# Kernel tuning notes

Hardware: AMD Instinct MI355X
Metric: run time of the kernel (lower is better)

The kernel has to match this reference:

```python
import jax, jax.numpy as jnp
import numpy as np

VOCAB = 32000
EMB = 512
UNITS = 1024
B, T = 128, 256


def setup_inputs() -> dict:
    key = jax.random.key(0)
    ks = jax.random.split(key, 9)
    s = 0.05
    return {
        "tokens": jax.random.randint(ks[0], (B, T), 0, VOCAB),
        "emb_table": jax.random.normal(ks[1], (VOCAB, EMB), jnp.float32) * s,
        "Wx_f": jax.random.normal(ks[2], (EMB, 3 * UNITS), jnp.float32) * s,
        "Wh_f": jax.random.normal(ks[3], (UNITS, 3 * UNITS), jnp.float32) * s,
        "b_f": jnp.zeros((2, 3 * UNITS), jnp.float32),  # [input_bias, recurrent_bias] (reset_after=True)
        "Wx_b": jax.random.normal(ks[4], (EMB, 3 * UNITS), jnp.float32) * s,
        "Wh_b": jax.random.normal(ks[5], (UNITS, 3 * UNITS), jnp.float32) * s,
        "b_b": jnp.zeros((2, 3 * UNITS), jnp.float32),
        "fc_W": jax.random.normal(ks[6], (2 * UNITS, UNITS), jnp.float32) * s,
        "fc_b": jnp.zeros((UNITS,), jnp.float32),
    }


def _gru_dir(x_proj, mask, Wh, b_rec, reverse):
    # x_proj: [B,T,3U] precomputed input projections (z|r|h gate order, Keras),
    # mask: [B,T] bool. Keras GRU v2 semantics: reset_after=True,
    # sigmoid recurrent activation, tanh activation; masked steps carry state.
    b, u = x_proj.shape[0], Wh.shape[0]

    def step(h, inputs):
        xp, m = inputs  # [B,3U], [B]
        rec = h @ Wh + b_rec  # [B,3U]
        xz, xr, xh = jnp.split(xp, 3, axis=-1)
        rz, rr, rh = jnp.split(rec, 3, axis=-1)
        z = jax.nn.sigmoid(xz + rz)
        r = jax.nn.sigmoid(xr + rr)
        hh = jnp.tanh(xh + r * rh)
        h_new = z * h + (1.0 - z) * hh
        h_new = jnp.where(m[:, None], h_new, h)
        return h_new, h_new

    h0 = jnp.zeros((b, u), x_proj.dtype)
    xs = (jnp.swapaxes(x_proj, 0, 1), jnp.swapaxes(mask, 0, 1))  # time-major
    h_last, outs = jax.lax.scan(step, h0, xs, reverse=reverse)
    return jnp.swapaxes(outs, 0, 1), h_last  # [B,T,U], [B,U]


def reference(tokens, emb_table, Wx_f, Wh_f, b_f, Wx_b, Wh_b, b_b, fc_W, fc_b):
    mask = tokens != 0  # Embedding(mask_zero=True)
    x = emb_table[tokens]  # [B,T,E]
    xp_f = x @ Wx_f + b_f[0]
    xp_b = x @ Wx_b + b_b[0]
    out_f, h_f = _gru_dir(xp_f, mask, Wh_f, b_f[1], reverse=False)
    out_b, h_b = _gru_dir(xp_b, mask, Wh_b, b_b[1], reverse=True)
    output = jnp.concatenate([out_f, out_b], axis=-1)  # [B,T,2U]
    hidden = jnp.concatenate([h_f, h_b], axis=-1) @ fc_W + fc_b  # [B,U]
    return output, hidden
```

## Files before the change

### kernel.cpp

```cpp
#include <hip/hip_runtime.h>


#define T_SEQ 256
#define BATCH 128
#define EMB_D 512
#define UNITS 1024
#define NROWS (BATCH * T_SEQ)
#define N3U 3072
#define N6U 6144
#define XT_STRIDE 786432
#define HSTR (BATCH * 2048)
#define HROT 16

#define SBAR()      __builtin_amdgcn_s_barrier()
#define SCHED0()    __builtin_amdgcn_sched_barrier(0)
#define WAIT_LGKM() asm volatile("s_waitcnt lgkmcnt(0)" ::: "memory")
#define WAIT_VM()   asm volatile("s_waitcnt vmcnt(0)" ::: "memory")

typedef __attribute__((ext_vector_type(8))) __bf16 bfv8;
typedef __attribute__((ext_vector_type(4))) float f32x4;

__device__ inline unsigned short f2bf(float f) {
  union { float f; unsigned int u; } x; x.f = f;
  unsigned int u = x.u;
  unsigned int r = (u + 0x7fffu + ((u >> 16) & 1u)) >> 16;
  return (unsigned short)r;
}
__device__ inline float bf2f(unsigned short h) {
  union { unsigned int u; float f; } x; x.u = ((unsigned int)h) << 16;
  return x.f;
}
__device__ inline f32x4 mfma16(bfv8 a, bfv8 b, f32x4 c) {
  return __builtin_amdgcn_mfma_f32_16x16x32_bf16(a, b, c, 0, 0, 0);
}
__device__ inline void gl_lds16(const unsigned short* g, unsigned short* l) {
  __builtin_amdgcn_global_load_lds(
      (const __attribute__((address_space(1))) void*)g,
      (__attribute__((address_space(3))) void*)l, 16, 0, 0);
}

__global__ __launch_bounds__(256) void k_transpose(const float* __restrict__ src,
                                                   unsigned short* __restrict__ dst,
                                                   int K, int N) {
  __shared__ float tile[32][33];
  int k0 = blockIdx.x * 32, n0 = blockIdx.y * 32;
  int tx = threadIdx.x & 31, ty = threadIdx.x >> 5;
#pragma unroll
  for (int i = 0; i < 4; ++i)
    tile[ty + i * 8][tx] = src[(size_t)(k0 + ty + i * 8) * N + n0 + tx];
  __syncthreads();
#pragma unroll
  for (int i = 0; i < 4; ++i)
    dst[(size_t)(n0 + ty + i * 8) * K + k0 + tx] = f2bf(tile[tx][ty + i * 8]);
}

__global__ __launch_bounds__(256) void k_gather(const int* __restrict__ tokens,
                                                const float* __restrict__ emb,
                                                unsigned short* __restrict__ Xbf) {
  int idx = blockIdx.x * 256 + threadIdx.x;
  int row = idx >> 7;
  int c4 = (idx & 127) * 4;
  int tok = tokens[row];
  float4 v = *(const float4*)(emb + (size_t)tok * EMB_D + c4);
  ushort4 p;
  p.x = f2bf(v.x); p.y = f2bf(v.y); p.z = f2bf(v.z); p.w = f2bf(v.w);
  *(ushort4*)(Xbf + (size_t)row * EMB_D + c4) = p;
}

__global__ __launch_bounds__(256) void k_bias(const float* __restrict__ bf_,
                                              const float* __restrict__ bb_,
                                              float* __restrict__ biasX,
                                              float* __restrict__ biasH) {
  int i = blockIdx.x * 256 + threadIdx.x;
  if (i >= N6U) return;
  if (i < N3U) { biasX[i] = bf_[i];        biasH[i] = bf_[N3U + i]; }
  else         { biasX[i] = bb_[i - N3U];  biasH[i] = bb_[i]; }
}

__global__ __launch_bounds__(256) void k_tokt(const int* __restrict__ tokens,
                                              int* __restrict__ tokT) {
  int i = blockIdx.x * 256 + threadIdx.x;
  int b = i >> 8, t = i & 255;
  tokT[t * BATCH + b] = tokens[i];
}

__global__ __launch_bounds__(256) void k_gemm(const unsigned short* __restrict__ A,
                                              const unsigned short* __restrict__ BT,
                                              const float* __restrict__ bias,
                                              void* __restrict__ C,
                                              int M, int N, int K, int mode) {
  __shared__ unsigned short As[128 * 32];
  __shared__ unsigned short Bs[128 * 32];
  const int mt = blockIdx.x, nt = blockIdx.y;
  const int tid = threadIdx.x;
  const int wid = tid >> 6, lane = tid & 63;
  const int wm = (wid >> 1) * 64, wn = (wid & 1) * 64;
  const int l15 = lane & 15, lk = (lane >> 4) * 8;

  f32x4 acc[4][4];
#pragma unroll
  for (int i = 0; i < 4; ++i)
#pragma unroll
    for (int j = 0; j < 4; ++j) acc[i][j] = (f32x4){0.f, 0.f, 0.f, 0.f};

  const int r = tid >> 2;
  const int cc = (tid & 3) * 8;
  const unsigned short* ga0 = A + (size_t)(mt * 128 + r) * K + cc;
  const unsigned short* ga1 = ga0 + (size_t)64 * K;
  const unsigned short* gb0 = BT + (size_t)(nt * 128 + r) * K + cc;
  const unsigned short* gb1 = gb0 + (size_t)64 * K;
  unsigned short* lA0 = As + r * 32 + cc;
  unsigned short* lA1 = As + (64 + r) * 32 + cc;
  unsigned short* lB0 = Bs + r * 32 + cc;
  unsigned short* lB1 = Bs + (64 + r) * 32 + cc;

  for (int k0 = 0; k0 < K; k0 += 32) {
    __syncthreads();
    gl_lds16(ga0 + k0, lA0);
    gl_lds16(ga1 + k0, lA1);
    gl_lds16(gb0 + k0, lB0);
    gl_lds16(gb1 + k0, lB1);
    __syncthreads();
    bfv8 af[4], bfr[4];
#pragma unroll
    for (int i = 0; i < 4; ++i) {
      af[i]  = *(const bfv8*)(As + (wm + i * 16 + l15) * 32 + lk);
      bfr[i] = *(const bfv8*)(Bs + (wn + i * 16 + l15) * 32 + lk);
    }
#pragma unroll
    for (int i = 0; i < 4; ++i)
#pragma unroll
      for (int j = 0; j < 4; ++j) acc[i][j] = mfma16(af[i], bfr[j], acc[i][j]);
  }

#pragma unroll
  for (int j = 0; j < 4; ++j) {
    const int col = nt * 128 + wn + j * 16 + l15;
    const float bv = bias[col];
    const int dirc = (col >= N3U) ? 1 : 0;
    const int cm = col - dirc * N3U;
    const int g = cm >> 10;
    const int uu = cm & 1023;
    const size_t cbase = (size_t)dirc * 393216 + (size_t)(uu >> 4) * 6144 +
                         (size_t)g * 16 + (uu & 15);
#pragma unroll
    for (int i = 0; i < 4; ++i) {
      const int row0 = mt * 128 + wm + i * 16 + (lane >> 4) * 4;
#pragma unroll
      for (int q = 0; q < 4; ++q) {
        const float v = acc[i][j][q] + bv;
        const int row = row0 + q;
        if (mode == 1) {
          ((float*)C)[(size_t)row * N + col] = v;
        } else {
          const int b = row >> 8, tt = row & 255;
          ((unsigned short*)C)[(size_t)tt * XT_STRIDE + cbase + (size_t)b * 48] = f2bf(v);
        }
      }
    }
  }
}

__global__ __launch_bounds__(256) void k_scan(const unsigned short* __restrict__ XPn,
                                              const unsigned short* __restrict__ WhT,
                                              const float* __restrict__ biasH,
                                              const int* __restrict__ tokT,
                                              unsigned short* __restrict__ hbR,
                                              float* __restrict__ out,
                                              unsigned int* __restrict__ bar) {
  __shared__ unsigned short Wl[3 * 128 * 16 * 8];
  __shared__ unsigned short xb[64 * 48];
  __shared__ int tkb[64];
  __shared__ unsigned short bounce[64 * 24];

  const int bid = blockIdx.x;
  const int grp = bid & 3;
  const int dir = grp >> 1;
  const int mg  = grp & 1;
  const int ut  = bid >> 2;
  const int u0 = ut * 16, m0 = mg * 64;
  const int sub = ut & 7;
  const int tid = threadIdx.x;

  for (int c = tid; c < 6144; c += 256) {
    const int g  = c >> 11;
    const int kb = (c >> 4) & 127;
    const int uu = c & 15;
    *(uint4*)(Wl + (((g << 7) | kb) * 16 + uu) * 8) =
        *(const uint4*)(WhT + (((size_t)(dir * N3U + (g << 10) + u0 + uu)) << 10) + (kb << 3));
  }

  const int lane = tid & 63, wid = tid >> 6;
  const int l15 = lane & 15, hi = lane >> 4;
  const size_t aoff = ((size_t)(m0 + wid * 16 + l15) << 11) + (dir << 10) + (hi << 3);
  const int u = u0 + l15;
  const float bz  = biasH[dir * N3U + u];
  const float brg = biasH[dir * N3U + 1024 + u];
  const float bhg = biasH[dir * N3U + 2048 + u];
  const int rb = wid * 16 + (hi << 2);
  const int ob = m0 + rb;
  const size_t woff = (dir << 10) + u;
  const int sr = tid >> 2, sc4 = (tid & 3) << 2;
  const size_t soff = ((size_t)(m0 + sr) << 11) + (dir << 10) + u0 + sc4;

  const unsigned short* xpb = XPn + (size_t)dir * 393216 + (size_t)ut * 6144 + (size_t)m0 * 48;

  unsigned long long pf0, pf1, pf2; int pft = 0;
  {
    const int t0 = dir ? (T_SEQ - 1) : 0;
    const unsigned long long* xs = (const unsigned long long*)(xpb + (size_t)t0 * XT_STRIDE);
    pf0 = xs[tid]; pf1 = xs[tid + 256]; pf2 = xs[tid + 512];
    if (tid < 64) pft = tokT[t0 * BATCH + m0 + tid];
  }

  float hreg[4] = {0.f, 0.f, 0.f, 0.f};
  float oreg[4];
  __syncthreads();

  for (int s = 0; s < T_SEQ; ++s) {
    const int t = dir ? (T_SEQ - 1 - s) : s;
    const unsigned short* hrd = hbR + (size_t)((s + HROT - 1) & (HROT - 1)) * HSTR;
    unsigned short* hwr       = hbR + (size_t)(s & (HROT - 1)) * HSTR;

    const unsigned short* ap = hrd + aoff;
    bfv8 hA[16], hB[16];
#pragma unroll
    for (int ks = 0; ks < 16; ++ks) {
      hA[ks] = *(const bfv8*)(ap + (ks << 6));
      hB[ks] = *(const bfv8*)(ap + (ks << 6) + 32);
    }

    {
      unsigned long long* xd = (unsigned long long*)xb;
      xd[tid] = pf0; xd[tid + 256] = pf1; xd[tid + 512] = pf2;
      if (tid < 64) tkb[tid] = pft;
    }
    WAIT_LGKM(); SCHED0(); SBAR(); SCHED0();

    float xz[4], xr[4], xh[4]; int tok[4];
#pragma unroll
    for (int q = 0; q < 4; ++q) {
      const int xo = (rb + q) * 48 + l15;
      xz[q] = bf2f(xb[xo]);
      xr[q] = bf2f(xb[xo + 16]);
      xh[q] = bf2f(xb[xo + 32]);
      tok[q] = tkb[rb + q];
    }

    if (s + 1 < T_SEQ) {
      const int tn = dir ? (T_SEQ - 2 - s) : (s + 1);
      const unsigned long long* xs = (const unsigned long long*)(xpb + (size_t)tn * XT_STRIDE);
      pf0 = xs[tid]; pf1 = xs[tid + 256]; pf2 = xs[tid + 512];
      if (tid < 64) pft = tokT[tn * BATCH + m0 + tid];
    }

    f32x4 az0 = {0.f,0.f,0.f,0.f}, az1 = az0, ar0 = az0, ar1 = az0, ah0 = az0, ah1 = az0;
#pragma unroll
    for (int ks = 0; ks < 16; ++ks) {
      const unsigned short* wp = Wl + (((ks << 3) + hi) * 16 + l15) * 8;
      bfv8 wz0 = *(const bfv8*)(wp);
      bfv8 wr0 = *(const bfv8*)(wp + (1 << 14));
      bfv8 wh0 = *(const bfv8*)(wp + (2 << 14));
      bfv8 wz1 = *(const bfv8*)(wp + 512);
      bfv8 wr1 = *(const bfv8*)(wp + (1 << 14) + 512);
      bfv8 wh1 = *(const bfv8*)(wp + (2 << 14) + 512);
      az0 = mfma16(hA[ks], wz0, az0); ar0 = mfma16(hA[ks], wr0, ar0); ah0 = mfma16(hA[ks], wh0, ah0);
      az1 = mfma16(hB[ks], wz1, az1); ar1 = mfma16(hB[ks], wr1, ar1); ah1 = mfma16(hB[ks], wh1, ah1);
    }
    f32x4 az = az0 + az1, ar = ar0 + ar1, ah = ah0 + ah1;

#pragma unroll
    for (int q = 0; q < 4; ++q) {
      const float z  = 1.f / (1.f + __expf(-(xz[q] + az[q] + bz)));
      const float r  = 1.f / (1.f + __expf(-(xr[q] + ar[q] + brg)));
      const float hh = tanhf(xh[q] + r * (ah[q] + bhg));
      float hn = z * hreg[q] + (1.f - z) * hh;
      if (tok[q] == 0) hn = hreg[q];
      hreg[q] = hn;
      oreg[q] = hn;
      bounce[(rb + q) * 24 + l15] = f2bf(hn);
    }

    WAIT_LGKM(); SCHED0(); SBAR(); SCHED0();
    {
      unsigned long long v = *(const unsigned long long*)(bounce + sr * 24 + sc4);
      __hip_atomic_store((unsigned long long*)(hwr + soff), v,
                         __ATOMIC_RELAXED, __HIP_MEMORY_SCOPE_AGENT);
    }

    if (s + 1 < T_SEQ) {
      WAIT_VM(); SCHED0(); SBAR(); SCHED0();
#pragma unroll
      for (int q = 0; q < 4; ++q)
        out[((size_t)((ob + q) * T_SEQ + t) << 11) + woff] = oreg[q];
      if (tid == 0)
        __hip_atomic_fetch_add(&bar[((grp << 3) | sub) << 6], 1u,
                               __ATOMIC_RELAXED, __HIP_MEMORY_SCOPE_AGENT);
      if (tid < 8) {
        const unsigned tgt = 8u * (unsigned)(s + 1);
        unsigned int* p = &bar[((grp << 3) | tid) << 6];
        while (__hip_atomic_load(p, __ATOMIC_RELAXED, __HIP_MEMORY_SCOPE_AGENT) < tgt)
          __builtin_amdgcn_s_sleep(2);
        if ((s & (HROT - 1)) == HROT - 1)
          __builtin_amdgcn_fence(__ATOMIC_ACQUIRE, "agent");
      }
      SBAR(); SCHED0();
    } else {
#pragma unroll
      for (int q = 0; q < 4; ++q)
        out[((size_t)((ob + q) * T_SEQ + t) << 11) + woff] = oreg[q];
    }
  }
}

extern "C" void kernel_launch(void* const* d_in, const int* in_sizes, int n_in,
                              void* d_out, int out_size, void* d_ws, size_t ws_size,
                              hipStream_t stream) {
  const int* tokens = (const int*)d_in[0];
  const float* emb  = (const float*)d_in[1];
  const float* Wx_f = (const float*)d_in[2];
  const float* Wh_f = (const float*)d_in[3];
  const float* b_f  = (const float*)d_in[4];
  const float* Wx_b = (const float*)d_in[5];
  const float* Wh_b = (const float*)d_in[6];
  const float* b_b  = (const float*)d_in[7];
  const float* fc_W = (const float*)d_in[8];
  const float* fc_b = (const float*)d_in[9];
  float* out = (float*)d_out;

  char* w = (char*)d_ws;
  unsigned short* XPn = (unsigned short*)w; w += (size_t)NROWS * N6U * 2;
  unsigned short* Xbf = (unsigned short*)w; w += (size_t)NROWS * EMB_D * 2;
  unsigned short* WxT = (unsigned short*)w; w += (size_t)N6U * EMB_D * 2;
  unsigned short* WhT = (unsigned short*)w; w += (size_t)N6U * UNITS * 2;
  unsigned short* fcWT = (unsigned short*)w; w += (size_t)UNITS * 2048 * 2;
  unsigned short* hbR = (unsigned short*)w; w += (size_t)HROT * HSTR * 2;
  float* biasX = (float*)w; w += N6U * 4;
  float* biasH = (float*)w; w += N6U * 4;
  int* tokT = (int*)w; w += NROWS * 4;
  unsigned int* bar = (unsigned int*)w; w += 2048 * sizeof(unsigned int);

  (void)hipMemsetAsync((void*)(hbR + (size_t)(HROT - 1) * HSTR), 0, (size_t)HSTR * 2, stream);
  (void)hipMemsetAsync((void*)bar, 0, 2048 * sizeof(unsigned int), stream);

  k_transpose<<<dim3(EMB_D / 32, N3U / 32), 256, 0, stream>>>(Wx_f, WxT, EMB_D, N3U);
  k_transpose<<<dim3(EMB_D / 32, N3U / 32), 256, 0, stream>>>(Wx_b, WxT + (size_t)N3U * EMB_D, EMB_D, N3U);
  k_transpose<<<dim3(UNITS / 32, N3U / 32), 256, 0, stream>>>(Wh_f, WhT, UNITS, N3U);
  k_transpose<<<dim3(UNITS / 32, N3U / 32), 256, 0, stream>>>(Wh_b, WhT + (size_t)N3U * UNITS, UNITS, N3U);
  k_transpose<<<dim3(2048 / 32, 1024 / 32), 256, 0, stream>>>(fc_W, fcWT, 2048, 1024);
  k_bias<<<24, 256, 0, stream>>>(b_f, b_b, biasX, biasH);
  k_tokt<<<NROWS / 256, 256, 0, stream>>>(tokens, tokT);
  k_gather<<<(NROWS * 128) / 256, 256, 0, stream>>>(tokens, emb, Xbf);

  k_gemm<<<dim3(NROWS / 128, N6U / 128), 256, 0, stream>>>(Xbf, WxT, biasX, XPn, NROWS, N6U, EMB_D, 0);

  k_scan<<<256, 256, 0, stream>>>(XPn, WhT, biasH, tokT, hbR, out, bar);

  k_gemm<<<dim3(1, 8), 256, 0, stream>>>(hbR + (size_t)(HROT - 1) * HSTR, fcWT, fc_b,
                                         out + (size_t)NROWS * 2048, BATCH, UNITS, 2048, 1);
}
```

Measured before the change: 2.497 ms.

## Split scan recurrent matmul K dimension across two wave groups with LDS reduction

```diff
diff --git a/kernel.cpp b/kernel.cpp
--- a/kernel.cpp
+++ b/kernel.cpp
@@ -161,7 +161,7 @@
   }
 }
 
-__global__ __launch_bounds__(256) void k_scan(const unsigned short* __restrict__ XPn,
+__global__ __launch_bounds__(512) void k_scan(const unsigned short* __restrict__ XPn,
                                               const unsigned short* __restrict__ WhT,
                                               const float* __restrict__ biasH,
                                               const int* __restrict__ tokT,
@@ -172,6 +172,7 @@
   __shared__ unsigned short xb[64 * 48];
   __shared__ int tkb[64];
   __shared__ unsigned short bounce[64 * 24];
+  __shared__ float red[4][64][13];
 
   const int bid = blockIdx.x;
   const int grp = bid & 3;
@@ -182,7 +183,7 @@
   const int sub = ut & 7;
   const int tid = threadIdx.x;
 
-  for (int c = tid; c < 6144; c += 256) {
+  for (int c = tid; c < 6144; c += 512) {
     const int g  = c >> 11;
     const int kb = (c >> 4) & 127;
     const int uu = c & 15;
@@ -191,13 +192,14 @@
   }
 
   const int lane = tid & 63, wid = tid >> 6;
+  const int wlo = wid & 3, kh = wid >> 2;
   const int l15 = lane & 15, hi = lane >> 4;
-  const size_t aoff = ((size_t)(m0 + wid * 16 + l15) << 11) + (dir << 10) + (hi << 3);
+  const size_t aoff = ((size_t)(m0 + wlo * 16 + l15) << 11) + (dir << 10) + (kh << 9) + (hi << 3);
   const int u = u0 + l15;
   const float bz  = biasH[dir * N3U + u];
   const float brg = biasH[dir * N3U + 1024 + u];
   const float bhg = biasH[dir * N3U + 2048 + u];
-  const int rb = wid * 16 + (hi << 2);
+  const int rb = wlo * 16 + (hi << 2);
   const int ob = m0 + rb;
   const size_t woff = (dir << 10) + u;
   const int sr = tid >> 2, sc4 = (tid & 3) << 2;
@@ -205,11 +207,12 @@
 
   const unsigned short* xpb = XPn + (size_t)dir * 393216 + (size_t)ut * 6144 + (size_t)m0 * 48;
 
-  unsigned long long pf0, pf1, pf2; int pft = 0;
+  unsigned long long pf0, pf1 = 0; int pft = 0;
   {
     const int t0 = dir ? (T_SEQ - 1) : 0;
     const unsigned long long* xs = (const unsigned long long*)(xpb + (size_t)t0 * XT_STRIDE);
-    pf0 = xs[tid]; pf1 = xs[tid + 256]; pf2 = xs[tid + 512];
+    pf0 = xs[tid];
+    if (tid < 256) pf1 = xs[tid + 512];
     if (tid < 64) pft = tokT[t0 * BATCH + m0 + tid];
   }
 
@@ -222,67 +225,84 @@
     const unsigned short* hrd = hbR + (size_t)((s + HROT - 1) & (HROT - 1)) * HSTR;
     unsigned short* hwr       = hbR + (size_t)(s & (HROT - 1)) * HSTR;
 
-    const unsigned short* ap = hrd + aoff;
-    bfv8 hA[16], hB[16];
-#pragma unroll
-    for (int ks = 0; ks < 16; ++ks) {
-      hA[ks] = *(const bfv8*)(ap + (ks << 6));
-      hB[ks] = *(const bfv8*)(ap + (ks << 6) + 32);
-    }
-
     {
       unsigned long long* xd = (unsigned long long*)xb;
-      xd[tid] = pf0; xd[tid + 256] = pf1; xd[tid + 512] = pf2;
+      xd[tid] = pf0;
+      if (tid < 256) xd[tid + 512] = pf1;
       if (tid < 64) tkb[tid] = pft;
     }
     WAIT_LGKM(); SCHED0(); SBAR(); SCHED0();
 
     float xz[4], xr[4], xh[4]; int tok[4];
-#pragma unroll
-    for (int q = 0; q < 4; ++q) {
-      const int xo = (rb + q) * 48 + l15;
-      xz[q] = bf2f(xb[xo]);
-      xr[q] = bf2f(xb[xo + 16]);
-      xh[q] = bf2f(xb[xo + 32]);
-      tok[q] = tkb[rb + q];
+    if (kh == 0) {
+#pragma unroll
+      for (int q = 0; q < 4; ++q) {
+        const int xo = (rb + q) * 48 + l15;
+        xz[q] = bf2f(xb[xo]);
+        xr[q] = bf2f(xb[xo + 16]);
+        xh[q] = bf2f(xb[xo + 32]);
+        tok[q] = tkb[rb + q];
+      }
     }
 
     if (s + 1 < T_SEQ) {
       const int tn = dir ? (T_SEQ - 2 - s) : (s + 1);
       const unsigned long long* xs = (const unsigned long long*)(xpb + (size_t)tn * XT_STRIDE);
-      pf0 = xs[tid]; pf1 = xs[tid + 256]; pf2 = xs[tid + 512];
+      pf0 = xs[tid];
+      if (tid < 256) pf1 = xs[tid + 512];
       if (tid < 64) pft = tokT[tn * BATCH + m0 + tid];
     }
 
+    const unsigned short* ap = hrd + aoff;
     f32x4 az0 = {0.f,0.f,0.f,0.f}, az1 = az0, ar0 = az0, ar1 = az0, ah0 = az0, ah1 = az0;
 #pragma unroll
-    for (int ks = 0; ks < 16; ++ks) {
-      const unsigned short* wp = Wl + (((ks << 3) + hi) * 16 + l15) * 8;
+    for (int ks = 0; ks < 8; ++ks) {
+      bfv8 a0 = *(const bfv8*)(ap + (ks << 6));
+      bfv8 a1 = *(const bfv8*)(ap + (ks << 6) + 32);
+      const unsigned short* wp = Wl + ((((kh << 6) + (ks << 3) + hi) * 16 + l15) * 8);
       bfv8 wz0 = *(const bfv8*)(wp);
       bfv8 wr0 = *(const bfv8*)(wp + (1 << 14));
       bfv8 wh0 = *(const bfv8*)(wp + (2 << 14));
       bfv8 wz1 = *(const bfv8*)(wp + 512);
       bfv8 wr1 = *(const bfv8*)(wp + (1 << 14) + 512);
       bfv8 wh1 = *(const bfv8*)(wp + (2 << 14) + 512);
-      az0 = mfma16(hA[ks], wz0, az0); ar0 = mfma16(hA[ks], wr0, ar0); ah0 = mfma16(hA[ks], wh0, ah0);
-      az1 = mfma16(hB[ks], wz1, az1); ar1 = mfma16(hB[ks], wr1, ar1); ah1 = mfma16(hB[ks], wh1, ah1);
+      az0 = mfma16(a0, wz0, az0); ar0 = mfma16(a0, wr0, ar0); ah0 = mfma16(a0, wh0, ah0);
+      az1 = mfma16(a1, wz1, az1); ar1 = mfma16(a1, wr1, ar1); ah1 = mfma16(a1, wh1, ah1);
     }
     f32x4 az = az0 + az1, ar = ar0 + ar1, ah = ah0 + ah1;
 
-#pragma unroll
-    for (int q = 0; q < 4; ++q) {
-      const float z  = 1.f / (1.f + __expf(-(xz[q] + az[q] + bz)));
-      const float r  = 1.f / (1.f + __expf(-(xr[q] + ar[q] + brg)));
-      const float hh = tanhf(xh[q] + r * (ah[q] + bhg));
-      float hn = z * hreg[q] + (1.f - z) * hh;
-      if (tok[q] == 0) hn = hreg[q];
-      hreg[q] = hn;
-      oreg[q] = hn;
-      bounce[(rb + q) * 24 + l15] = f2bf(hn);
-    }
-
+    if (kh == 1) {
+#pragma unroll
+      for (int j = 0; j < 4; ++j) {
+        red[wlo][lane][j]     = az[j];
+        red[wlo][lane][4 + j] = ar[j];
+        red[wlo][lane][8 + j] = ah[j];
+      }
+    }
     WAIT_LGKM(); SCHED0(); SBAR(); SCHED0();
-    {
+
+    if (kh == 0) {
+#pragma unroll
+      for (int j = 0; j < 4; ++j) {
+        az[j] += red[wlo][lane][j];
+        ar[j] += red[wlo][lane][4 + j];
+        ah[j] += red[wlo][lane][8 + j];
+      }
+#pragma unroll
+      for (int q = 0; q < 4; ++q) {
+        const float z  = 1.f / (1.f + __expf(-(xz[q] + az[q] + bz)));
+        const float r  = 1.f / (1.f + __expf(-(xr[q] + ar[q] + brg)));
+        const float hh = tanhf(xh[q] + r * (ah[q] + bhg));
+        float hn = z * hreg[q] + (1.f - z) * hh;
+        if (tok[q] == 0) hn = hreg[q];
+        hreg[q] = hn;
+        oreg[q] = hn;
+        bounce[(rb + q) * 24 + l15] = f2bf(hn);
+      }
+    }
+
+    WAIT_LGKM(); SCHED0(); SBAR(); SCHED0();
+    if (tid < 256) {
       unsigned long long v = *(const unsigned long long*)(bounce + sr * 24 + sc4);
       __hip_atomic_store((unsigned long long*)(hwr + soff), v,
                          __ATOMIC_RELAXED, __HIP_MEMORY_SCOPE_AGENT);
@@ -290,9 +310,11 @@
 
     if (s + 1 < T_SEQ) {
       WAIT_VM(); SCHED0(); SBAR(); SCHED0();
-#pragma unroll
-      for (int q = 0; q < 4; ++q)
-        out[((size_t)((ob + q) * T_SEQ + t) << 11) + woff] = oreg[q];
+      if (kh == 0) {
+#pragma unroll
+        for (int q = 0; q < 4; ++q)
+          out[((size_t)((ob + q) * T_SEQ + t) << 11) + woff] = oreg[q];
+      }
       if (tid == 0)
         __hip_atomic_fetch_add(&bar[((grp << 3) | sub) << 6], 1u,
                                __ATOMIC_RELAXED, __HIP_MEMORY_SCOPE_AGENT);
@@ -306,9 +328,11 @@
       }
       SBAR(); SCHED0();
     } else {
-#pragma unroll
-      for (int q = 0; q < 4; ++q)
-        out[((size_t)((ob + q) * T_SEQ + t) << 11) + woff] = oreg[q];
+      if (kh == 0) {
+#pragma unroll
+        for (int q = 0; q < 4; ++q)
+          out[((size_t)((ob + q) * T_SEQ + t) << 11) + woff] = oreg[q];
+      }
     }
   }
 }
@@ -354,7 +378,7 @@
 
   k_gemm<<<dim3(NROWS / 128, N6U / 128), 256, 0, stream>>>(Xbf, WxT, biasX, XPn, NROWS, N6U, EMB_D, 0);
 
-  k_scan<<<256, 256, 0, stream>>>(XPn, WhT, biasH, tokT, hbR, out, bar);
+  k_scan<<<256, 512, 0, stream>>>(XPn, WhT, biasH, tokT, hbR, out, bar);
 
   k_gemm<<<dim3(1, 8), 256, 0, stream>>>(hbR + (size_t)(HROT - 1) * HSTR, fcWT, fc_b,
                                          out + (size_t)NROWS * 2048, BATCH, UNITS, 2048, 1);
```

After: 2.459 ms. Within noise of the previous version (-1.5%).
